# Kernel tuning notes

Hardware: AMD Instinct MI355X
Metric: run time of the kernel (lower is better)

Reference implementation:

```python
import jax, jax.numpy as jnp
import numpy as np

# Dimensions: B walkers, NSPIN spins, NPS electrons per spin, DFEAT equivariant
# feature dim, NION ions, DSP spatial dim.
B, NSPIN, NPS, DFEAT, NION, DSP = 2048, 2, 8, 256, 4, 3


def setup_inputs() -> dict:
    key = jax.random.key(0)
    k0, k1, k2, k3, k4, k5 = jax.random.split(key, 6)
    eq_inputs = jax.random.normal(k0, (B, NSPIN * NPS, DFEAT), jnp.float32)
    r_ei = jax.random.normal(k1, (B, NSPIN * NPS, NION, DSP), jnp.float32)
    # Linear part of the orbitals: maps pair features (2*DFEAT) -> NPS orbitals per spin.
    W = jax.random.normal(k2, (NSPIN, 2 * DFEAT, NPS), jnp.float32) / np.sqrt(2.0 * DFEAT)
    b = 0.01 * jax.random.normal(k3, (NSPIN, NPS), jnp.float32)
    # Anisotropic decay: one DSPxDSP matrix per (spin, orbital, ion), near identity.
    env_dim = jnp.eye(DSP, dtype=jnp.float32)[None, None, None] + 0.05 * jax.random.normal(
        k4, (NSPIN, NPS, NION, DSP, DSP), jnp.float32
    )
    # Linear combination over ions per (spin, ion, orbital).
    env_ion = jnp.full((NSPIN, NION, NPS), 1.0 / NION, jnp.float32) + 0.05 * jax.random.normal(
        k5, (NSPIN, NION, NPS), jnp.float32
    )
    return {
        "eq_inputs": eq_inputs,
        "r_ei": r_ei,
        "W": W,
        "b": b,
        "env_dim": env_dim,
        "env_ion": env_ion,
    }


def reference(eq_inputs, r_ei, W, b, env_dim, env_ion):
    Bsz = eq_inputs.shape[0]
    # Split equally into spins: (B, NSPIN, NPS, DFEAT)
    x = eq_inputs.reshape(Bsz, NSPIN, NPS, DFEAT)
    # Doubly-equivariant pair features: concat(x_i, x_j) -> (B, S, n, n, 2d)
    shp = (Bsz, NSPIN, NPS, NPS, DFEAT)
    xi = jnp.broadcast_to(x[:, :, :, None, :], shp)
    xj = jnpp_concat = jnp.broadcast_to(x[:, :, None, :, :], shp)
    pairs = jnp.concatenate([xi, xj], axis=-1)
    # Linear part of the per-particle orbital matrices: (B, S, i, j, k)
    orb = jnp.einsum("bsijf,sfk->bsijk", pairs, W) + b[None, :, None, None, :]
    # Anisotropic exponential envelopes on the orbital-evaluated electron j:
    # env_{b,s,j,k} = sum_a env_ion[s,a,k] * exp(-||env_dim[s,k,a] @ r_ei[b,s,j,a]||)
    r = r_ei.reshape(Bsz, NSPIN, NPS, NION, DSP)
    scaled = jnp.einsum("bsjad,skade->bsjkae", r, env_dim)  # (B,S,j,k,a,e)
    dist = jnp.linalg.norm(scaled, axis=-1)  # (B,S,j,k,a)
    env = jnp.einsum("bsjka,sak->bsjk", jnp.exp(-dist), env_ion)
    orb = orb * env[:, :, None, :, :]
    # Per-particle determinants over the (j,k) axes: (B, S, n)
    dets = jnp.linalg.det(orb)[..., None]  # (B, S, n, 1)
    # Per-spin list, each (B, n, 1)
    return (dets[:, 0], dets[:, 1])
```

## Files before the change

kernel.cpp:

```cpp
#include <hip/hip_runtime.h>

#define BATCH 2048
#define NPS 8
#define DFEAT 256

__global__ __launch_bounds__(512) void ppdet_kernel(
    const float* __restrict__ eq,
    const float* __restrict__ r_ei,
    const float* __restrict__ W,
    const float* __restrict__ bias,
    const float* __restrict__ env_dim,
    const float* __restrict__ env_ion,
    float* __restrict__ out)
{
    __shared__ __align__(16) float part[8 * 64 * 16];
    __shared__ __align__(16) float AB[64 * 16];
    __shared__ __align__(16) float envl[512];

    const int tid = threadIdx.x;
    const int bid = blockIdx.x;
    const int s  = bid & 1;
    const int b0 = (bid >> 1) * 8;

    const int wq   = __builtin_amdgcn_readfirstlane(tid >> 6);
    const int lane = tid & 63;
    const int wl   = lane >> 3, ii = lane & 7;

    const float* wb1 = W + s * 4096 + wq * (32 * NPS);
    const size_t grow = (size_t)(b0 + wl) * 16 + s * 8 + ii;
    const float* xrow = eq + grow * DFEAT + wq * 32;

    float4 xv[8];
#pragma unroll
    for (int u = 0; u < 8; ++u) xv[u] = ((const float4*)xrow)[u];

    float acc[16];
#pragma unroll
    for (int k = 0; k < 16; ++k) acc[k] = 0.f;

#pragma unroll
    for (int u = 0; u < 8; ++u) {
        const float* wr = wb1 + u * 32;
        float xs0 = xv[u].x, xs1 = xv[u].y, xs2 = xv[u].z, xs3 = xv[u].w;
#pragma unroll
        for (int c = 0; c < 4; ++c) {
            float xc = (c == 0) ? xs0 : (c == 1) ? xs1 : (c == 2) ? xs2 : xs3;
#pragma unroll
            for (int k = 0; k < 8; ++k) {
                acc[k]     = fmaf(xc, wr[c * 8 + k],        acc[k]);
                acc[8 + k] = fmaf(xc, wr[2048 + c * 8 + k], acc[8 + k]);
            }
        }
    }

    {
        float* pb = part + (wq * 64 + lane) * 16;
        const int sw = (lane >> 1) & 3;
#pragma unroll
        for (int kg = 0; kg < 4; ++kg) {
            int slot = kg ^ sw;
            float4 v = make_float4(acc[kg * 4], acc[kg * 4 + 1],
                                   acc[kg * 4 + 2], acc[kg * 4 + 3]);
            *(float4*)(pb + slot * 4) = v;
        }
    }

    {
        const int w = tid >> 6, k = (tid >> 3) & 7, j = tid & 7;
        const size_t rrow = ((size_t)(b0 + w) * 16 + s * 8 + j) * 12;
        const float4* rp = (const float4*)(r_ei + rrow);
        float4 ra = rp[0], rb = rp[1], rc = rp[2];
        float rr[12] = {ra.x, ra.y, ra.z, ra.w, rb.x, rb.y, rb.z, rb.w,
                        rc.x, rc.y, rc.z, rc.w};
        float e = 0.f;
#pragma unroll
        for (int a = 0; a < 4; ++a) {
            const float* Md = env_dim + ((size_t)(s * 8 + k) * 4 + a) * 9;
            float r0 = rr[a * 3], r1 = rr[a * 3 + 1], r2 = rr[a * 3 + 2];
            float e0 = r0 * Md[0] + r1 * Md[3] + r2 * Md[6];
            float e1 = r0 * Md[1] + r1 * Md[4] + r2 * Md[7];
            float e2 = r0 * Md[2] + r1 * Md[5] + r2 * Md[8];
            float dist = sqrtf(e0 * e0 + e1 * e1 + e2 * e2);
            e = fmaf(env_ion[(s * 4 + a) * 8 + k], __expf(-dist), e);
        }
        envl[w * 64 + j * 8 + k] = e;
    }

    __syncthreads();

    if (tid < 256) {
        const int row = tid >> 2, sl = tid & 3;
        const int g = sl ^ ((row >> 1) & 3);
        float4 sum = make_float4(0.f, 0.f, 0.f, 0.f);
#pragma unroll
        for (int q2 = 0; q2 < 8; ++q2) {
            float4 v = *(const float4*)(part + (q2 * 64 + row) * 16 + sl * 4);
            sum.x += v.x; sum.y += v.y; sum.z += v.z; sum.w += v.w;
        }
        if (g < 2) {
            sum.x += bias[s * 8 + g * 4];
            sum.y += bias[s * 8 + g * 4 + 1];
            sum.z += bias[s * 8 + g * 4 + 2];
            sum.w += bias[s * 8 + g * 4 + 3];
        }
        *(float4*)(AB + row * 16 + g * 4) = sum;
    }

    __syncthreads();

    {
        const int grp = tid >> 3;
        const int w = grp >> 3, i = grp & 7, j = tid & 7;
        const float* Arow = AB + (w * 8 + i) * 16;
        const float* Brow = AB + (w * 8 + j) * 16 + 8;
        const float* Erow = envl + w * 64 + j * 8;
        float m[8];
#pragma unroll
        for (int k = 0; k < 8; ++k) m[k] = (Arow[k] + Brow[k]) * Erow[k];

        float det_acc = 1.f;
        bool elim = false;
        int pis[8];
#pragma unroll
        for (int p = 0; p < 8; ++p) {
            float aval = elim ? -1.f : fabsf(m[p]);
            int aidx = j;
#pragma unroll
            for (int mb = 1; mb < 8; mb <<= 1) {
                float ov = __shfl_xor(aval, mb);
                int   oi = __shfl_xor(aidx, mb);
                bool take = (ov > aval) || (ov == aval && oi < aidx);
                aval = take ? ov : aval;
                aidx = take ? oi : aidx;
            }
            pis[p] = aidx;
            const int src = (tid & 56) | aidx;
            float prow[8];
#pragma unroll
            for (int k = 0; k < 8; ++k) prow[k] = __shfl(m[k], src);
            det_acc *= prow[p];
            elim = elim || (j == aidx);
            float f = (!elim && aval > 0.f)
                        ? m[p] * __builtin_amdgcn_rcpf(prow[p]) : 0.f;
#pragma unroll
            for (int k = 0; k < 8; ++k) m[k] = fmaf(-f, prow[k], m[k]);
        }
        int inv = 0;
#pragma unroll
        for (int a = 0; a < 8; ++a)
#pragma unroll
            for (int b2 = a + 1; b2 < 8; ++b2) inv += (pis[a] > pis[b2]) ? 1 : 0;
        if (j == 0) {
            float dd = (inv & 1) ? -det_acc : det_acc;
            out[(size_t)s * (BATCH * NPS) + (size_t)(b0 + w) * NPS + i] = dd;
        }
    }
}

extern "C" void kernel_launch(void* const* d_in, const int* in_sizes, int n_in,
                              void* d_out, int out_size, void* d_ws, size_t ws_size,
                              hipStream_t stream) {
    const float* eq      = (const float*)d_in[0];
    const float* r_ei    = (const float*)d_in[1];
    const float* W       = (const float*)d_in[2];
    const float* bias    = (const float*)d_in[3];
    const float* env_dim = (const float*)d_in[4];
    const float* env_ion = (const float*)d_in[5];
    float* out = (float*)d_out;

    ppdet_kernel<<<512, 512, 0, stream>>>(eq, r_ei, W, bias, env_dim, env_ion, out);
}
```

Before: 17.21 us.

## Stage eq rows through transposed swizzled LDS for coalesced global loads

Each wave previously loaded strided 32-float chunks of eight different rows straight from global memory. Now each wave loads full 256-float rows with coalesced float4 reads and writes them transposed into an XOR-swizzled shared buffer. The GEMM phase then reads its feature slices from LDS. The shared buffer is reused for the partial sums, which adds two extra barriers and a larger LDS footprint (about 72KB), and that may lower occupancy.

```diff
diff --git a/kernel.cpp b/kernel.cpp
--- a/kernel.cpp
+++ b/kernel.cpp
@@ -13,9 +13,11 @@
     const float* __restrict__ env_ion,
     float* __restrict__ out)
 {
-    __shared__ __align__(16) float part[8 * 64 * 16];
-    __shared__ __align__(16) float AB[64 * 16];
-    __shared__ __align__(16) float envl[512];
+    __shared__ __align__(16) float smem[16384 + 1024 + 512];
+    float* XT   = smem;
+    float* part = smem;
+    float* AB   = smem + 16384;
+    float* envl = smem + 16384 + 1024;
 
     const int tid = threadIdx.x;
     const int bid = blockIdx.x;
@@ -24,44 +26,16 @@
 
     const int wq   = __builtin_amdgcn_readfirstlane(tid >> 6);
     const int lane = tid & 63;
-    const int wl   = lane >> 3, ii = lane & 7;
-
-    const float* wb1 = W + s * 4096 + wq * (32 * NPS);
-    const size_t grow = (size_t)(b0 + wl) * 16 + s * 8 + ii;
-    const float* xrow = eq + grow * DFEAT + wq * 32;
-
-    float4 xv[8];
-#pragma unroll
-    for (int u = 0; u < 8; ++u) xv[u] = ((const float4*)xrow)[u];
-
-    float acc[16];
-#pragma unroll
-    for (int k = 0; k < 16; ++k) acc[k] = 0.f;
-
-#pragma unroll
-    for (int u = 0; u < 8; ++u) {
-        const float* wr = wb1 + u * 32;
-        float xs0 = xv[u].x, xs1 = xv[u].y, xs2 = xv[u].z, xs3 = xv[u].w;
-#pragma unroll
-        for (int c = 0; c < 4; ++c) {
-            float xc = (c == 0) ? xs0 : (c == 1) ? xs1 : (c == 2) ? xs2 : xs3;
-#pragma unroll
-            for (int k = 0; k < 8; ++k) {
-                acc[k]     = fmaf(xc, wr[c * 8 + k],        acc[k]);
-                acc[8 + k] = fmaf(xc, wr[2048 + c * 8 + k], acc[8 + k]);
-            }
-        }
-    }
 
     {
-        float* pb = part + (wq * 64 + lane) * 16;
-        const int sw = (lane >> 1) & 3;
+        const float* gbase = eq + ((size_t)(b0 + wq) * 16 + s * 8) * DFEAT;
+        const int msk = lane & 31;
 #pragma unroll
-        for (int kg = 0; kg < 4; ++kg) {
-            int slot = kg ^ sw;
-            float4 v = make_float4(acc[kg * 4], acc[kg * 4 + 1],
-                                   acc[kg * 4 + 2], acc[kg * 4 + 3]);
-            *(float4*)(pb + slot * 4) = v;
+        for (int ii = 0; ii < 8; ++ii) {
+            float4 v = ((const float4*)(gbase + ii * DFEAT))[lane];
+            const int r = wq * 8 + ii;
+            float* dst = XT + (size_t)(lane * 4) * 64 + (r ^ msk);
+            dst[0] = v.x; dst[64] = v.y; dst[128] = v.z; dst[192] = v.w;
         }
     }
 
@@ -84,6 +58,44 @@
             e = fmaf(env_ion[(s * 4 + a) * 8 + k], __expf(-dist), e);
         }
         envl[w * 64 + j * 8 + k] = e;
+    }
+
+    __syncthreads();
+
+    float acc[16];
+#pragma unroll
+    for (int k = 0; k < 16; ++k) acc[k] = 0.f;
+
+    const float* wb1 = W + s * 4096 + wq * 256;
+#pragma unroll
+    for (int g8 = 0; g8 < 8; ++g8) {
+        const int g = wq * 8 + g8;
+        const float* xb = XT + (size_t)(4 * g) * 64 + (lane ^ (g & 31));
+        float xs0 = xb[0], xs1 = xb[64], xs2 = xb[128], xs3 = xb[192];
+        const float* wr = wb1 + g8 * 32;
+#pragma unroll
+        for (int c = 0; c < 4; ++c) {
+            float xc = (c == 0) ? xs0 : (c == 1) ? xs1 : (c == 2) ? xs2 : xs3;
+#pragma unroll
+            for (int k = 0; k < 8; ++k) {
+                acc[k]     = fmaf(xc, wr[c * 8 + k],        acc[k]);
+                acc[8 + k] = fmaf(xc, wr[2048 + c * 8 + k], acc[8 + k]);
+            }
+        }
+    }
+
+    __syncthreads();
+
+    {
+        float* pb = part + (wq * 64 + lane) * 16;
+        const int sw = (lane >> 1) & 3;
+#pragma unroll
+        for (int kg = 0; kg < 4; ++kg) {
+            int slot = kg ^ sw;
+            float4 v = make_float4(acc[kg * 4], acc[kg * 4 + 1],
+                                   acc[kg * 4 + 2], acc[kg * 4 + 3]);
+            *(float4*)(pb + slot * 4) = v;
+        }
     }
 
     __syncthreads();
```

After: 16.93 us. Within noise of the previous version (-1.6%).
